# Performance work log

Measured on AMD Instinct MI355X. Metric: run time of the kernel, lower is better.

The kernel has to match this reference:

```python
import jax, jax.numpy as jnp
import numpy as np

B, C, H, W = 8, 128, 128, 128
PLANES, K, STRIDE, PAD = 128, 3, 1, 1
BN_EPS = 1e-5


def setup_inputs() -> dict:
    key = jax.random.key(0)
    k1, k2, k3, k4 = jax.random.split(key, 4)
    x = jax.random.normal(k1, (B, C, H, W), jnp.float32)
    # ConvOffset2D: Conv2d(C, 2C, 3, pad=1, bias=False), weights ~ N(0, 0.01)
    w_off = jax.random.normal(k2, (2 * C, C, 3, 3), jnp.float32) * 0.01
    w_conv = jax.random.normal(k3, (PLANES, C, K, K), jnp.float32) * 0.05
    b_conv = jax.random.normal(k4, (PLANES,), jnp.float32) * 0.01
    gamma = jnp.ones((PLANES,), jnp.float32)
    beta = jnp.zeros((PLANES,), jnp.float32)
    return {"x": x, "w_off": w_off, "w_conv": w_conv, "b_conv": b_conv,
            "gamma": gamma, "beta": beta}


def _conv2d(x, w, stride, pad):
    return jax.lax.conv_general_dilated(
        x, w, window_strides=(stride, stride),
        padding=[(pad, pad), (pad, pad)],
        dimension_numbers=("NCHW", "OIHW", "NCHW"))


def _deform_sample(x, offsets):
    """x: (B,C,H,W); offsets: (B,2C,H,W) -> bilinear offset-sampled (B,C,H,W).
    Faithful to ConvOffset2D: raw reshape (b,2c,h,w) -> (b*c, h*w, 2),
    coords = offsets + meshgrid(i,j), clamp, bilinear interp."""
    b, c, h, w = x.shape
    off = offsets.reshape(b * c, h * w, 2)              # quirky but faithful reshape
    grid = jnp.stack(jnp.meshgrid(jnp.arange(h, dtype=x.dtype),
                                  jnp.arange(w, dtype=x.dtype),
                                  indexing="ij"), axis=-1).reshape(1, h * w, 2)
    coords = off + grid                                  # (b*c, h*w, 2)
    yc = jnp.clip(coords[..., 0], 0.0, h - 1.0)
    xc = jnp.clip(coords[..., 1], 0.0, w - 1.0)
    y0, y1 = jnp.floor(yc), jnp.ceil(yc)
    x0, x1 = jnp.floor(xc), jnp.ceil(xc)
    img = x.reshape(b * c, h * w)

    def gather(yy, xx):
        idx = (yy * w + xx).astype(jnp.int32)
        return jnp.take_along_axis(img, idx, axis=1)

    v_lt = gather(y0, x0)
    v_rb = gather(y1, x1)
    v_lb = gather(y0, x1)
    v_rt = gather(y1, x0)
    dy = yc - y0
    dx = xc - x0
    v_t = v_lt + (v_rt - v_lt) * dy   # interp along height
    v_b = v_lb + (v_rb - v_lb) * dy
    out = v_t + (v_b - v_t) * dx      # interp along width
    return out.reshape(b, c, h, w)


def reference(x, w_off, w_conv, b_conv, gamma, beta):
    offsets = _conv2d(x, w_off, 1, 1)                    # (B, 2C, H, W)
    x_off = _deform_sample(x, offsets)                   # (B, C, H, W)
    y = _conv2d(x_off, w_conv, STRIDE, PAD) + b_conv[None, :, None, None]
    y = jax.nn.relu(y)
    # BatchNorm2d in training mode: batch statistics, biased variance
    mean = y.mean(axis=(0, 2, 3), keepdims=True)
    var = jnp.square(y - mean).mean(axis=(0, 2, 3), keepdims=True)
    y = (y - mean) * jax.lax.rsqrt(var + BN_EPS)
    return y * gamma[None, :, None, None] + beta[None, :, None, None]
```

## Files before the change

kernel.cpp:

```cpp
#include <hip/hip_runtime.h>

#define B_   8
#define C_   128
#define H_   128
#define W_   128
#define HW_  16384

typedef short v8s __attribute__((ext_vector_type(8)));
typedef float v4f __attribute__((ext_vector_type(4)));

#define ROWB 4160

__device__ __forceinline__ float bf2f(unsigned short u) {
  unsigned int v = ((unsigned int)u) << 16;
  float f; __builtin_memcpy(&f, &v, 4); return f;
}
__device__ __forceinline__ unsigned short f2us(float f) {
  unsigned int u; __builtin_memcpy(&u, &f, 4);
  u += 0x7fffu + ((u >> 16) & 1u);
  return (unsigned short)(u >> 16);
}

__global__ __launch_bounds__(256) void prep(const float* __restrict__ x,
                                            unsigned short* __restrict__ xt,
                                            const float* __restrict__ w_off,
                                            const float* __restrict__ w_conv,
                                            unsigned short* __restrict__ pack_off,
                                            unsigned short* __restrict__ pack_main,
                                            uint4* __restrict__ zb) {
  __shared__ alignas(16) unsigned short t[32 * 132];
  const int bid = blockIdx.x, tid = threadIdx.x;
  if (bid < 4096) {
    const int j0 = (bid & 3) * 32, i = (bid >> 2) & 127, b = bid >> 9;
    for (int e = tid; e < 128 * 32; e += 256) {
      int c = e >> 5, jj = e & 31;
      float v = x[((b * C_ + c) * H_ + i) * W_ + j0 + jj];
      t[jj * 132 + c] = f2us(v);
    }
    __syncthreads();
    for (int f = tid; f < 1024; f += 256) {
      int cg = f >> 7, g = f & 127;
      int j = g >> 2, c4 = (g & 3) << 2;
      uint2 v = *(const uint2*)&t[j * 132 + cg * 16 + c4];
      *(uint2*)(xt + ((size_t)(b * 8 + cg) * HW_ + i * W_ + j0 + j) * 16 + c4) = v;
    }
    return;
  }
  const int pb = bid - 4096;
  if (pb == 0) zb[tid] = (uint4){0u, 0u, 0u, 0u};
  const float* w;
  unsigned short* pack;
  int G, idx;
  if (pb < 1280) { w = w_off;  pack = pack_off;  G = 16; idx = pb * 256 + tid; }
  else           { w = w_conv; pack = pack_main; G = 8;  idx = (pb - 1280) * 256 + tid; }
  if (idx >= 20480 * G) return;
  int j  = idx & 7;
  int l  = (idx >> 3) & 63;
  int g  = (idx >> 9) % G;
  int t2 = idx / (512 * G);
  int pp = t2 % 5;
  int cc = t2 / 5;
  int oc = g * 16 + (l & 15);
  int kk = ((l >> 4) << 3) + j;
  int ic = (cc << 4) + (kk & 15);
  int rs = pp * 2 + (kk >> 4);
  float v = (rs < 9) ? w[(oc * C_ + ic) * 9 + rs] : 0.f;
  pack[idx] = f2us(v);
}

template <int MODE, int G>
__global__ __launch_bounds__(256, 4) void conv_gemm(const unsigned short* __restrict__ xt,
                                                    const unsigned short* __restrict__ pack,
                                                    const float* __restrict__ bias,
                                                    const char* __restrict__ zb,
                                                    unsigned short* __restrict__ outp,
                                                    float* __restrict__ ps) {
  __shared__ alignas(16) char rawb[3 * ROWB];
  __shared__ float bs1[128], bs2[128];

  const int nb = blockIdx.x;
  int b, i, mt;
  {
    int xcd = nb & 7, r = nb >> 3;
    if (MODE == 0) { b = r >> 5; mt = (r >> 4) & 1; i = xcd * 16 + (r & 15); }
    else           { b = r >> 4; mt = 0;            i = xcd * 16 + (r & 15); }
  }
  const int tid  = threadIdx.x;
  const int lane = tid & 63, wid = tid >> 6;
  const int q = lane >> 4, n = lane & 15;
  const int wm = wid & 1, wn = wid >> 1;

  if (MODE == 1 && tid < 128) { bs1[tid] = 0.f; bs2[tid] = 0.f; }
  if (tid < 12) {
    int r = tid >> 2, rem = tid & 3, side = rem >> 1, h = rem & 1;
    *(uint4*)(rawb + r * ROWB + (side ? 129 * 32 : 0) + h * 16) = (uint4){0u,0u,0u,0u};
  }

  int boff[5];
#pragma unroll
  for (int pp = 0; pp < 5; ++pp) {
    int rs = pp * 2 + (q >> 1);
    if (rs > 8) rs = 8;
    int r = (rs >= 6) ? 2 : ((rs >= 3) ? 1 : 0);
    int s = rs - r * 3;
    boff[pp] = r * ROWB + s * 32 + (q & 1) * 16;
  }
  const int pcol = (wn * 64 + n) * 32;

  v4f acc[4][4];
#pragma unroll
  for (int a = 0; a < 4; ++a)
#pragma unroll
    for (int c = 0; c < 4; ++c) acc[a][c] = (v4f){0.f, 0.f, 0.f, 0.f};

  const v8s* packv = (const v8s*)pack;
  const int gbase = mt * 8 + wm * 4;

  for (int cc = 0; cc < 8; ++cc) {
    __syncthreads();
    const char* ccbase = (const char*)xt + (size_t)(b * 8 + cc) * (HW_ * 32);
#pragma unroll
    for (int t = 0; t < 3; ++t) {
      int c = wid * 3 + t, r = c >> 2, k = c & 3;
      int ii = i + r - 1;
      const char* src = ((unsigned)ii < 128u)
                          ? ccbase + ii * 4096 + k * 1024 + lane * 16
                          : zb + lane * 16;
      __builtin_amdgcn_global_load_lds(
          (const __attribute__((address_space(1))) unsigned int*)src,
          (__attribute__((address_space(3))) unsigned int*)(rawb + r * ROWB + 32 + k * 1024),
          16, 0, 0);
    }
    __syncthreads();

#pragma unroll
    for (int pp = 0; pp < 5; ++pp) {
      const v8s* ap = packv + ((cc * 5 + pp) * G + gbase) * 64 + lane;
      v8s Af[4];
#pragma unroll
      for (int fm = 0; fm < 4; ++fm) Af[fm] = ap[fm * 64];
      v8s Bf[4];
#pragma unroll
      for (int fn = 0; fn < 4; ++fn)
        Bf[fn] = *(const v8s*)(rawb + boff[pp] + pcol + fn * 512);
#pragma unroll
      for (int fm = 0; fm < 4; ++fm) {
#pragma unroll
        for (int fn = 0; fn < 4; ++fn)
          acc[fm][fn] = __builtin_amdgcn_mfma_f32_16x16x32_bf16(Af[fm], Bf[fn],
                                                                acc[fm][fn], 0, 0, 0);
      }
    }
  }

  const int OC = G * 16;
  const int ob = (b * OC + mt * 128 + wm * 64) * HW_ + i * W_ + wn * 64;

  if (MODE == 0) {
#pragma unroll
    for (int fm = 0; fm < 4; ++fm)
#pragma unroll
      for (int fn = 0; fn < 4; ++fn)
#pragma unroll
        for (int rr = 0; rr < 4; ++rr)
          outp[ob + (fm * 16 + q * 4 + rr) * HW_ + fn * 16 + n] = f2us(acc[fm][fn][rr]);
  } else {
    float bv[4][4], s1a[4][4], s2a[4][4];
#pragma unroll
    for (int fm = 0; fm < 4; ++fm)
#pragma unroll
      for (int rr = 0; rr < 4; ++rr) {
        bv[fm][rr] = bias[wm * 64 + fm * 16 + q * 4 + rr];
        s1a[fm][rr] = 0.f; s2a[fm][rr] = 0.f;
      }
#pragma unroll
    for (int fm = 0; fm < 4; ++fm)
#pragma unroll
      for (int fn = 0; fn < 4; ++fn)
#pragma unroll
        for (int rr = 0; rr < 4; ++rr) {
          float v = acc[fm][fn][rr] + bv[fm][rr];
          v = fmaxf(v, 0.f);
          outp[ob + (fm * 16 + q * 4 + rr) * HW_ + fn * 16 + n] = f2us(v);
          s1a[fm][rr] += v; s2a[fm][rr] += v * v;
        }
#pragma unroll
    for (int fm = 0; fm < 4; ++fm)
#pragma unroll
      for (int rr = 0; rr < 4; ++rr) {
        float s1 = s1a[fm][rr], s2 = s2a[fm][rr];
#pragma unroll
        for (int m = 1; m < 16; m <<= 1) {
          s1 += __shfl_xor(s1, m);
          s2 += __shfl_xor(s2, m);
        }
        if (n == 0) {
          atomicAdd(&bs1[wm * 64 + fm * 16 + q * 4 + rr], s1);
          atomicAdd(&bs2[wm * 64 + fm * 16 + q * 4 + rr], s2);
        }
      }
    __syncthreads();
    if (tid < 128) {
      ps[nb * 128 + tid]          = bs1[tid];
      ps[131072 + nb * 128 + tid] = bs2[tid];
    }
  }
}

__global__ __launch_bounds__(256) void deform_t(const float* __restrict__ x,
                                                const unsigned short* __restrict__ offs,
                                                unsigned short* __restrict__ xofft) {
  __shared__ alignas(16) unsigned short t[128 * 132];
  const int i = blockIdx.x, b = blockIdx.y;
  const int tid = threadIdx.x;
  for (int e = tid; e < 16384; e += 256) {
    int c = e >> 7, j = e & 127;
    int qpix = (i << 7) + j;
    int oidx = (b << 22) + (c << 15) + 2 * qpix;
    unsigned int pr = *(const unsigned int*)(offs + oidx);
    float oy = bf2f((unsigned short)(pr & 0xffffu));
    float ox = bf2f((unsigned short)(pr >> 16));
    float yc = fminf(fmaxf(oy + (float)i, 0.f), 127.f);
    float xc = fminf(fmaxf(ox + (float)j, 0.f), 127.f);
    float y0f = floorf(yc), y1f = ceilf(yc);
    float x0f = floorf(xc), x1f = ceilf(xc);
    int y0 = (int)y0f, y1 = (int)y1f, x0 = (int)x0f, x1 = (int)x1f;
    const float* img = x + ((b * C_ + c) << 14);
    float v_lt = img[y0 * W_ + x0];
    float v_rb = img[y1 * W_ + x1];
    float v_lb = img[y0 * W_ + x1];
    float v_rt = img[y1 * W_ + x0];
    float dy = yc - y0f, dx = xc - x0f;
    float v_t = v_lt + (v_rt - v_lt) * dy;
    float v_b = v_lb + (v_rb - v_lb) * dy;
    float o   = v_t + (v_b - v_t) * dx;
    t[j * 132 + c] = f2us(o);
  }
  __syncthreads();
  for (int f = tid; f < 4096; f += 256) {
    int cg = f >> 9, g = f & 511;
    int j = g >> 2, c4 = (g & 3) << 2;
    uint2 v = *(const uint2*)&t[j * 132 + cg * 16 + c4];
    *(uint2*)(xofft + ((size_t)(b * 8 + cg) * HW_ + i * W_ + j) * 16 + c4) = v;
  }
}

__global__ __launch_bounds__(256) void bn_finalize(const float* __restrict__ ps,
                                                   const float* __restrict__ gamma,
                                                   const float* __restrict__ beta,
                                                   float* __restrict__ stats) {
  const int c = blockIdx.x, tid = threadIdx.x;
  float s1 = 0.f, s2 = 0.f;
  for (int k = tid; k < 1024; k += 256) {
    s1 += ps[k * 128 + c];
    s2 += ps[131072 + k * 128 + c];
  }
#pragma unroll
  for (int m = 32; m > 0; m >>= 1) {
    s1 += __shfl_down(s1, m);
    s2 += __shfl_down(s2, m);
  }
  __shared__ float l1[4], l2[4];
  int wid = tid >> 6;
  if ((tid & 63) == 0) { l1[wid] = s1; l2[wid] = s2; }
  __syncthreads();
  if (tid == 0) {
    s1 = l1[0] + l1[1] + l1[2] + l1[3];
    s2 = l2[0] + l2[1] + l2[2] + l2[3];
    const float invn = 1.f / 131072.f;
    float mean = s1 * invn;
    float var  = s2 * invn - mean * mean;
    float inv  = rsqrtf(var + 1e-5f);
    float sc = gamma[c] * inv;
    stats[c]       = sc;
    stats[128 + c] = beta[c] - mean * sc;
  }
}

__global__ __launch_bounds__(256) void bn_apply(const unsigned short* __restrict__ y,
                                                const float* __restrict__ stats,
                                                float* __restrict__ out) {
  int gid = blockIdx.x * 256 + threadIdx.x;
  int base = gid << 3;
  int c = (base >> 14) & 127;
  float sc = stats[c], sh = stats[128 + c];
  uint4 u = *(const uint4*)(y + base);
  const unsigned short* us = (const unsigned short*)&u;
  float4 o0, o1;
  o0.x = bf2f(us[0]) * sc + sh;  o0.y = bf2f(us[1]) * sc + sh;
  o0.z = bf2f(us[2]) * sc + sh;  o0.w = bf2f(us[3]) * sc + sh;
  o1.x = bf2f(us[4]) * sc + sh;  o1.y = bf2f(us[5]) * sc + sh;
  o1.z = bf2f(us[6]) * sc + sh;  o1.w = bf2f(us[7]) * sc + sh;
  ((float4*)out)[gid * 2]     = o0;
  ((float4*)out)[gid * 2 + 1] = o1;
}

extern "C" void kernel_launch(void* const* d_in, const int* in_sizes, int n_in,
                              void* d_out, int out_size, void* d_ws, size_t ws_size,
                              hipStream_t stream) {
  const float* x      = (const float*)d_in[0];
  const float* w_off  = (const float*)d_in[1];
  const float* w_conv = (const float*)d_in[2];
  const float* b_conv = (const float*)d_in[3];
  const float* gamma  = (const float*)d_in[4];
  const float* beta   = (const float*)d_in[5];
  float* out = (float*)d_out;

  char* ws = (char*)d_ws;
  unsigned short* x_t    = (unsigned short*)ws;
  unsigned short* xoff_t = (unsigned short*)ws;
  unsigned short* offs = (unsigned short*)(ws + 33554432);
  unsigned short* yws  = (unsigned short*)(ws + 33554432);
  float* ps    = (float*)(ws + 67108864);
  float* stats = (float*)(ws + 68157440);
  unsigned short* pack_off  = (unsigned short*)(ws + 100663296);
  unsigned short* pack_main = (unsigned short*)(ws + 101318656);
  char* zb = ws + 101646336;

  prep<<<6016, 256, 0, stream>>>(x, x_t, w_off, w_conv, pack_off, pack_main,
                                 (uint4*)zb);
  conv_gemm<0, 16><<<2048, 256, 0, stream>>>(x_t, pack_off, nullptr, zb, offs, nullptr);
  deform_t<<<dim3(128, 8), 256, 0, stream>>>(x, offs, xoff_t);
  conv_gemm<1, 8><<<1024, 256, 0, stream>>>(xoff_t, pack_main, b_conv, zb, yws, ps);
  bn_finalize<<<128, 256, 0, stream>>>(ps, gamma, beta, stats);
  bn_apply<<<8192, 256, 0, stream>>>(yws, stats, out);
}
```

Before: 311.8 us.

## Process channel-chunk pairs per stage to remove zero-padded K slots in conv GEMM

The implicit-GEMM conv now loads two 16-channel chunks (six input rows) into LDS per iteration and packs the K dimension as 18 taps split into 9 MFMA steps. The old layout used 5 steps per 9 taps, so one step in five was zero padding. The change removes that wasted MFMA work and halves the number of sync/load phases. In exchange it doubles LDS per block, which may reduce occupancy, and the weight-pack indexing gets more complex.

```diff
diff --git a/kernel.cpp b/kernel.cpp
--- a/kernel.cpp
+++ b/kernel.cpp
@@ -51,21 +51,21 @@
   const float* w;
   unsigned short* pack;
   int G, idx;
-  if (pb < 1280) { w = w_off;  pack = pack_off;  G = 16; idx = pb * 256 + tid; }
-  else           { w = w_conv; pack = pack_main; G = 8;  idx = (pb - 1280) * 256 + tid; }
-  if (idx >= 20480 * G) return;
+  if (pb < 1152) { w = w_off;  pack = pack_off;  G = 16; idx = pb * 256 + tid; }
+  else           { w = w_conv; pack = pack_main; G = 8;  idx = (pb - 1152) * 256 + tid; }
+  if (idx >= 18432 * G) return;
   int j  = idx & 7;
   int l  = (idx >> 3) & 63;
   int g  = (idx >> 9) % G;
   int t2 = idx / (512 * G);
-  int pp = t2 % 5;
-  int cc = t2 / 5;
+  int pp = t2 % 9;
+  int P  = t2 / 9;
   int oc = g * 16 + (l & 15);
   int kk = ((l >> 4) << 3) + j;
-  int ic = (cc << 4) + (kk & 15);
-  int rs = pp * 2 + (kk >> 4);
-  float v = (rs < 9) ? w[(oc * C_ + ic) * 9 + rs] : 0.f;
-  pack[idx] = f2us(v);
+  int gk = pp * 2 + (kk >> 4);
+  int ccl = gk / 9, rs = gk - ccl * 9;
+  int ic = (P * 2 + ccl) * 16 + (kk & 15);
+  pack[idx] = f2us(w[(oc * C_ + ic) * 9 + rs]);
 }
 
 template <int MODE, int G>
@@ -75,7 +75,7 @@
                                                     const char* __restrict__ zb,
                                                     unsigned short* __restrict__ outp,
                                                     float* __restrict__ ps) {
-  __shared__ alignas(16) char rawb[3 * ROWB];
+  __shared__ alignas(16) char rawb[6 * ROWB];
   __shared__ float bs1[128], bs2[128];
 
   const int nb = blockIdx.x;
@@ -91,18 +91,17 @@
   const int wm = wid & 1, wn = wid >> 1;
 
   if (MODE == 1 && tid < 128) { bs1[tid] = 0.f; bs2[tid] = 0.f; }
-  if (tid < 12) {
+  if (tid < 24) {
     int r = tid >> 2, rem = tid & 3, side = rem >> 1, h = rem & 1;
     *(uint4*)(rawb + r * ROWB + (side ? 129 * 32 : 0) + h * 16) = (uint4){0u,0u,0u,0u};
   }
 
-  int boff[5];
-#pragma unroll
-  for (int pp = 0; pp < 5; ++pp) {
-    int rs = pp * 2 + (q >> 1);
-    if (rs > 8) rs = 8;
-    int r = (rs >= 6) ? 2 : ((rs >= 3) ? 1 : 0);
-    int s = rs - r * 3;
+  int boff[9];
+#pragma unroll
+  for (int pp = 0; pp < 9; ++pp) {
+    int gk = pp * 2 + (q >> 1);
+    int ccl = gk / 9, rs = gk - ccl * 9;
+    int r = ccl * 3 + rs / 3, s = rs % 3;
     boff[pp] = r * ROWB + s * 32 + (q & 1) * 16;
   }
   const int pcol = (wn * 64 + n) * 32;
@@ -116,26 +115,28 @@
   const v8s* packv = (const v8s*)pack;
   const int gbase = mt * 8 + wm * 4;
 
-  for (int cc = 0; cc < 8; ++cc) {
+  for (int P = 0; P < 4; ++P) {
     __syncthreads();
-    const char* ccbase = (const char*)xt + (size_t)(b * 8 + cc) * (HW_ * 32);
-#pragma unroll
-    for (int t = 0; t < 3; ++t) {
-      int c = wid * 3 + t, r = c >> 2, k = c & 3;
+    const char* pbase = (const char*)xt + (size_t)(b * 8 + P * 2) * (HW_ * 32);
+#pragma unroll
+    for (int t = 0; t < 6; ++t) {
+      int c = wid * 6 + t;
+      int ccl = c >= 12, c2 = c - ccl * 12;
+      int r = c2 >> 2, k = c2 & 3;
       int ii = i + r - 1;
       const char* src = ((unsigned)ii < 128u)
-                          ? ccbase + ii * 4096 + k * 1024 + lane * 16
+                          ? pbase + (size_t)ccl * (HW_ * 32) + ii * 4096 + k * 1024 + lane * 16
                           : zb + lane * 16;
       __builtin_amdgcn_global_load_lds(
           (const __attribute__((address_space(1))) unsigned int*)src,
-          (__attribute__((address_space(3))) unsigned int*)(rawb + r * ROWB + 32 + k * 1024),
+          (__attribute__((address_space(3))) unsigned int*)(rawb + (ccl * 3 + r) * ROWB + 32 + k * 1024),
           16, 0, 0);
     }
     __syncthreads();
 
 #pragma unroll
-    for (int pp = 0; pp < 5; ++pp) {
-      const v8s* ap = packv + ((cc * 5 + pp) * G + gbase) * 64 + lane;
+    for (int pp = 0; pp < 9; ++pp) {
+      const v8s* ap = packv + ((P * 9 + pp) * G + gbase) * 64 + lane;
       v8s Af[4];
 #pragma unroll
       for (int fm = 0; fm < 4; ++fm) Af[fm] = ap[fm * 64];
@@ -317,7 +318,7 @@
   unsigned short* pack_main = (unsigned short*)(ws + 101318656);
   char* zb = ws + 101646336;
 
-  prep<<<6016, 256, 0, stream>>>(x, x_t, w_off, w_conv, pack_off, pack_main,
+  prep<<<5824, 256, 0, stream>>>(x, x_t, w_off, w_conv, pack_off, pack_main,
                                  (uint4*)zb);
   conv_gemm<0, 16><<<2048, 256, 0, stream>>>(x_t, pack_off, nullptr, zb, offs, nullptr);
   deform_t<<<dim3(128, 8), 256, 0, stream>>>(x, offs, xoff_t);
```

New measurement: 348.6 us. 11.8% more time.
